# Performance work log

Hardware: AMD Instinct MI355X
Metric: run time of the kernel (lower is better)

## Reference

```python
import jax, jax.numpy as jnp
import numpy as np

A = 5.0  # smoothness parameter 'a'

def setup_inputs() -> dict:
    key = jax.random.key(0)
    kx, kw = jax.random.split(key)
    x = jax.random.uniform(kx, (1024, 512), dtype=jnp.float32)
    weight = jax.random.uniform(kw, (512, 512), dtype=jnp.float32)
    return {"x": x, "weight": weight}

def reference(x, weight):
    # inner: [batch, in, out] broadcast min
    inner = jnp.minimum(x[..., None], weight[None])
    # smooth union (smooth max) over the 'in' dim: logsumexp(a*z)/a
    smooth = jax.scipy.special.logsumexp(A * inner, axis=-2) / A
    hard = jnp.max(inner, axis=-2)
    # straight-through: forward value = hard, gradient flows through smooth
    return jax.lax.stop_gradient(hard - smooth) + smooth
```

## Files before the change

kernel.cpp:

```cpp
#include <hip/hip_runtime.h>


typedef _Float16 h2 __attribute__((ext_vector_type(2)));
typedef unsigned int uint32;

#define MDIM 1024
#define KDIM 512
#define NDIM 512
#define K2   (KDIM / 2)
#define MB   8
#define NT   256
#define NWAVE 8
#define KP   (K2 / NWAVE)

__device__ __forceinline__ uint32 pkmin(uint32 a, uint32 b) {
    uint32 d;
    asm("v_pk_min_f16 %0, %1, %2" : "=v"(d) : "v"(a), "v"(b));
    return d;
}
__device__ __forceinline__ uint32 pkmax(uint32 a, uint32 b) {
    uint32 d;
    asm("v_pk_max_f16 %0, %1, %2" : "=v"(d) : "v"(a), "v"(b));
    return d;
}

__global__ __launch_bounds__(512) void pack_f16(const float* __restrict__ x,
                                                const float* __restrict__ w,
                                                uint32* __restrict__ xp,
                                                uint32* __restrict__ wp)
{
    const int b = blockIdx.x, tid = threadIdx.x;
    if (b < 256) {
        const int idx = b * 512 + tid;
        const int k2 = idx >> 9, n = idx & 511;
        h2 v;
        v[0] = (_Float16)w[(size_t)(2 * k2) * NDIM + n];
        v[1] = (_Float16)w[(size_t)(2 * k2 + 1) * NDIM + n];
        wp[idx] = __builtin_bit_cast(uint32, v);
    } else {
        const int idx = (b - 256) * 512 + tid;
        const float2 f = ((const float2*)x)[idx];
        h2 v;
        v[0] = (_Float16)f.x;
        v[1] = (_Float16)f.y;
        xp[idx] = __builtin_bit_cast(uint32, v);
    }
}

__global__ __launch_bounds__(512, 2) void tropical_r16(
    const uint32* __restrict__ xp,
    const uint32* __restrict__ wp,
    float* __restrict__ out)
{
    const int tid  = threadIdx.x;
    const int lane = tid & 63;
    const int wv   = tid >> 6;
    const int m0   = blockIdx.x * MB;
    const int n0   = blockIdx.y * NT;
    const int kp0  = __builtin_amdgcn_readfirstlane(wv * KP);

    __shared__ float red[NWAVE][MB][NT];

    const uint4* __restrict__ wb =
        (const uint4*)(wp + (size_t)kp0 * NDIM + n0) + lane;
    const uint32* __restrict__ xr0 = xp + (size_t)m0 * K2 + kp0;

    uint32 acc[MB][4];
#pragma unroll
    for (int r = 0; r < MB; ++r)
#pragma unroll
        for (int j = 0; j < 4; ++j) acc[r][j] = 0u;

    uint4 A = wb[0], B = wb[(size_t)128];

#pragma unroll 2
    for (int i = 0; i < KP; ++i) {
        uint4 C;
        if (i + 2 < KP) C = wb[(size_t)(i + 2) * 128];
#pragma unroll
        for (int r = 0; r < MB; ++r) {
            const uint32 xv = xr0[(size_t)r * K2 + i];
            acc[r][0] = pkmax(acc[r][0], pkmin(xv, A.x));
            acc[r][1] = pkmax(acc[r][1], pkmin(xv, A.y));
            acc[r][2] = pkmax(acc[r][2], pkmin(xv, A.z));
            acc[r][3] = pkmax(acc[r][3], pkmin(xv, A.w));
        }
        A = B; B = C;
    }

#pragma unroll
    for (int r = 0; r < MB; ++r) {
        float4 v;
        {
            h2 a0 = __builtin_bit_cast(h2, acc[r][0]);
            h2 a1 = __builtin_bit_cast(h2, acc[r][1]);
            h2 a2 = __builtin_bit_cast(h2, acc[r][2]);
            h2 a3 = __builtin_bit_cast(h2, acc[r][3]);
            v.x = fmaxf((float)a0[0], (float)a0[1]);
            v.y = fmaxf((float)a1[0], (float)a1[1]);
            v.z = fmaxf((float)a2[0], (float)a2[1]);
            v.w = fmaxf((float)a3[0], (float)a3[1]);
        }
        ((float4*)&red[wv][r][0])[lane] = v;
    }
    __syncthreads();

    {
        const int r  = tid >> 6;
        const int c4 = tid & 63;
        float4 v = ((const float4*)&red[0][r][0])[c4];
#pragma unroll
        for (int q = 1; q < NWAVE; ++q) {
            float4 u = ((const float4*)&red[q][r][0])[c4];
            v.x = fmaxf(v.x, u.x); v.y = fmaxf(v.y, u.y);
            v.z = fmaxf(v.z, u.z); v.w = fmaxf(v.w, u.w);
        }
        *(float4*)(out + (size_t)(m0 + r) * NDIM + n0 + 4 * c4) = v;
    }
}

extern "C" void kernel_launch(void* const* d_in, const int* in_sizes, int n_in,
                              void* d_out, int out_size, void* d_ws, size_t ws_size,
                              hipStream_t stream) {
    const float* x = (const float*)d_in[0];
    const float* w = (const float*)d_in[1];
    float* out = (float*)d_out;

    uint32* xp = (uint32*)d_ws;
    uint32* wp = xp + (size_t)MDIM * K2;

    pack_f16<<<dim3(768), dim3(512), 0, stream>>>(x, w, xp, wp);
    tropical_r16<<<dim3(MDIM / MB, NDIM / NT), dim3(512), 0, stream>>>(xp, wp, out);
}
```

Before: 72.14 us.

## Transpose packed x for contiguous scalar loads and retile to 16x128 blocks

The pack kernel now writes the f16-packed x in k-major order. This lets each block read a contiguous run of 16 rows per k step through uniform scalar loads, and the inline asm forces the x operand of v_pk_min_f16 into an SGPR. The output tile changes from 8 rows by 256 columns to 16 rows by 128 columns, so each lane holds 2 packed columns instead of 4. The goal is fewer weight bytes per x value and cheaper wide scalar x fetches. In exchange, the transposing pack reads x with a large stride and is uncoalesced, which adds cost to the pre-pass.

Result: slower. 74.76 us (+3.6%).

```diff
diff --git a/kernel.cpp b/kernel.cpp
--- a/kernel.cpp
+++ b/kernel.cpp
@@ -7,15 +7,15 @@
 #define MDIM 1024
 #define KDIM 512
 #define NDIM 512
-#define K2   (KDIM / 2)
-#define MB   8
-#define NT   256
+#define K2   256
+#define MB   16
+#define NT   128
 #define NWAVE 8
-#define KP   (K2 / NWAVE)
+#define KP   32
 
-__device__ __forceinline__ uint32 pkmin(uint32 a, uint32 b) {
+__device__ __forceinline__ uint32 pkmin_sv(uint32 s, uint32 v) {
     uint32 d;
-    asm("v_pk_min_f16 %0, %1, %2" : "=v"(d) : "v"(a), "v"(b));
+    asm("v_pk_min_f16 %0, %1, %2" : "=v"(d) : "s"(s), "v"(v));
     return d;
 }
 __device__ __forceinline__ uint32 pkmax(uint32 a, uint32 b) {
@@ -24,10 +24,10 @@
     return d;
 }
 
-__global__ __launch_bounds__(512) void pack_f16(const float* __restrict__ x,
-                                                const float* __restrict__ w,
-                                                uint32* __restrict__ xp,
-                                                uint32* __restrict__ wp)
+__global__ __launch_bounds__(512) void pack_t(const float* __restrict__ x,
+                                              const float* __restrict__ w,
+                                              uint32* __restrict__ xpT,
+                                              uint32* __restrict__ wp)
 {
     const int b = blockIdx.x, tid = threadIdx.x;
     if (b < 256) {
@@ -39,16 +39,17 @@
         wp[idx] = __builtin_bit_cast(uint32, v);
     } else {
         const int idx = (b - 256) * 512 + tid;
-        const float2 f = ((const float2*)x)[idx];
+        const int k2 = idx >> 10, m = idx & 1023;
+        const float2 f = ((const float2*)x)[(size_t)m * K2 + k2];
         h2 v;
         v[0] = (_Float16)f.x;
         v[1] = (_Float16)f.y;
-        xp[idx] = __builtin_bit_cast(uint32, v);
+        xpT[idx] = __builtin_bit_cast(uint32, v);
     }
 }
 
-__global__ __launch_bounds__(512, 2) void tropical_r16(
-    const uint32* __restrict__ xp,
+__global__ __launch_bounds__(512, 2) void tropical_r17(
+    const uint32* __restrict__ xpT,
     const uint32* __restrict__ wp,
     float* __restrict__ out)
 {
@@ -61,53 +62,44 @@
 
     __shared__ float red[NWAVE][MB][NT];
 
-    const uint4* __restrict__ wb =
-        (const uint4*)(wp + (size_t)kp0 * NDIM + n0) + lane;
-    const uint32* __restrict__ xr0 = xp + (size_t)m0 * K2 + kp0;
+    const uint32* __restrict__ xs = xpT + (size_t)kp0 * MDIM + m0;
+    const uint2* __restrict__ wb2 =
+        (const uint2*)(wp + (size_t)kp0 * NDIM + n0) + lane;
 
-    uint32 acc[MB][4];
+    uint32 acc[MB][2];
 #pragma unroll
-    for (int r = 0; r < MB; ++r)
-#pragma unroll
-        for (int j = 0; j < 4; ++j) acc[r][j] = 0u;
+    for (int r = 0; r < MB; ++r) { acc[r][0] = 0u; acc[r][1] = 0u; }
 
-    uint4 A = wb[0], B = wb[(size_t)128];
+    uint2 A = wb2[0], B = wb2[256];
 
 #pragma unroll 2
     for (int i = 0; i < KP; ++i) {
-        uint4 C;
-        if (i + 2 < KP) C = wb[(size_t)(i + 2) * 128];
+        uint2 C;
+        if (i + 2 < KP) C = wb2[(size_t)(i + 2) * 256];
+        const uint32* __restrict__ xr = xs + (size_t)i * MDIM;
 #pragma unroll
         for (int r = 0; r < MB; ++r) {
-            const uint32 xv = xr0[(size_t)r * K2 + i];
-            acc[r][0] = pkmax(acc[r][0], pkmin(xv, A.x));
-            acc[r][1] = pkmax(acc[r][1], pkmin(xv, A.y));
-            acc[r][2] = pkmax(acc[r][2], pkmin(xv, A.z));
-            acc[r][3] = pkmax(acc[r][3], pkmin(xv, A.w));
+            const uint32 xv = xr[r];
+            acc[r][0] = pkmax(acc[r][0], pkmin_sv(xv, A.x));
+            acc[r][1] = pkmax(acc[r][1], pkmin_sv(xv, A.y));
         }
         A = B; B = C;
     }
 
 #pragma unroll
     for (int r = 0; r < MB; ++r) {
-        float4 v;
-        {
-            h2 a0 = __builtin_bit_cast(h2, acc[r][0]);
-            h2 a1 = __builtin_bit_cast(h2, acc[r][1]);
-            h2 a2 = __builtin_bit_cast(h2, acc[r][2]);
-            h2 a3 = __builtin_bit_cast(h2, acc[r][3]);
-            v.x = fmaxf((float)a0[0], (float)a0[1]);
-            v.y = fmaxf((float)a1[0], (float)a1[1]);
-            v.z = fmaxf((float)a2[0], (float)a2[1]);
-            v.w = fmaxf((float)a3[0], (float)a3[1]);
-        }
-        ((float4*)&red[wv][r][0])[lane] = v;
+        h2 a0 = __builtin_bit_cast(h2, acc[r][0]);
+        h2 a1 = __builtin_bit_cast(h2, acc[r][1]);
+        float2 v;
+        v.x = fmaxf((float)a0[0], (float)a0[1]);
+        v.y = fmaxf((float)a1[0], (float)a1[1]);
+        ((float2*)&red[wv][r][0])[lane] = v;
     }
     __syncthreads();
 
     {
-        const int r  = tid >> 6;
-        const int c4 = tid & 63;
+        const int r  = tid >> 5;
+        const int c4 = tid & 31;
         float4 v = ((const float4*)&red[0][r][0])[c4];
 #pragma unroll
         for (int q = 1; q < NWAVE; ++q) {
@@ -126,9 +118,9 @@
     const float* w = (const float*)d_in[1];
     float* out = (float*)d_out;
 
-    uint32* xp = (uint32*)d_ws;
-    uint32* wp = xp + (size_t)MDIM * K2;
+    uint32* xpT = (uint32*)d_ws;
+    uint32* wp  = xpT + (size_t)K2 * MDIM;
 
-    pack_f16<<<dim3(768), dim3(512), 0, stream>>>(x, w, xp, wp);
-    tropical_r16<<<dim3(MDIM / MB, NDIM / NT), dim3(512), 0, stream>>>(xp, wp, out);
+    pack_t<<<dim3(768), dim3(512), 0, stream>>>(x, w, xpT, wp);
+    tropical_r17<<<dim3(MDIM / MB, NDIM / NT), dim3(512), 0, stream>>>(xpT, wp, out);
 }
```

## Fuse fp16 packing into tropical kernel, reading fp32 inputs directly

Applied to the files above, without the earlier changes.

Drops the separate pack_f16 kernel and converts fp32 x and weight to packed fp16 inside the main min-max loop using v_cvt_pk_f16_f32. This removes one kernel launch and a global write/read round trip of the packed buffers. In exchange each block loads twice as many bytes of weight and x, and does redundant conversions in the inner loop across blocks.

Result: no change. 72.10 us (-0.1%).

```diff
diff --git a/kernel.cpp b/kernel.cpp
--- a/kernel.cpp
+++ b/kernel.cpp
@@ -7,11 +7,10 @@
 #define MDIM 1024
 #define KDIM 512
 #define NDIM 512
-#define K2   (KDIM / 2)
-#define MB   8
-#define NT   256
+#define MB 8
+#define NT 256
+#define KW 64
 #define NWAVE 8
-#define KP   (K2 / NWAVE)
 
 __device__ __forceinline__ uint32 pkmin(uint32 a, uint32 b) {
     uint32 d;
@@ -23,33 +22,15 @@
     asm("v_pk_max_f16 %0, %1, %2" : "=v"(d) : "v"(a), "v"(b));
     return d;
 }
-
-__global__ __launch_bounds__(512) void pack_f16(const float* __restrict__ x,
-                                                const float* __restrict__ w,
-                                                uint32* __restrict__ xp,
-                                                uint32* __restrict__ wp)
-{
-    const int b = blockIdx.x, tid = threadIdx.x;
-    if (b < 256) {
-        const int idx = b * 512 + tid;
-        const int k2 = idx >> 9, n = idx & 511;
-        h2 v;
-        v[0] = (_Float16)w[(size_t)(2 * k2) * NDIM + n];
-        v[1] = (_Float16)w[(size_t)(2 * k2 + 1) * NDIM + n];
-        wp[idx] = __builtin_bit_cast(uint32, v);
-    } else {
-        const int idx = (b - 256) * 512 + tid;
-        const float2 f = ((const float2*)x)[idx];
-        h2 v;
-        v[0] = (_Float16)f.x;
-        v[1] = (_Float16)f.y;
-        xp[idx] = __builtin_bit_cast(uint32, v);
-    }
+__device__ __forceinline__ uint32 cvt_pk(float lo, float hi) {
+    uint32 d;
+    asm("v_cvt_pk_f16_f32 %0, %1, %2" : "=v"(d) : "v"(lo), "v"(hi));
+    return d;
 }
 
-__global__ __launch_bounds__(512, 2) void tropical_r16(
-    const uint32* __restrict__ xp,
-    const uint32* __restrict__ wp,
+__global__ __launch_bounds__(512, 2) void tropical_r18(
+    const float* __restrict__ x,
+    const float* __restrict__ w,
     float* __restrict__ out)
 {
     const int tid  = threadIdx.x;
@@ -57,13 +38,13 @@
     const int wv   = tid >> 6;
     const int m0   = blockIdx.x * MB;
     const int n0   = blockIdx.y * NT;
-    const int kp0  = __builtin_amdgcn_readfirstlane(wv * KP);
+    const int k0   = __builtin_amdgcn_readfirstlane(wv * KW);
 
     __shared__ float red[NWAVE][MB][NT];
 
-    const uint4* __restrict__ wb =
-        (const uint4*)(wp + (size_t)kp0 * NDIM + n0) + lane;
-    const uint32* __restrict__ xr0 = xp + (size_t)m0 * K2 + kp0;
+    const float4* __restrict__ wf =
+        (const float4*)(w + (size_t)k0 * NDIM + n0) + lane;
+    const float* __restrict__ xs = x + (size_t)m0 * KDIM + k0;
 
     uint32 acc[MB][4];
 #pragma unroll
@@ -71,36 +52,44 @@
 #pragma unroll
         for (int j = 0; j < 4; ++j) acc[r][j] = 0u;
 
-    uint4 A = wb[0], B = wb[(size_t)128];
+    float4 A0 = wf[0], A1 = wf[128];
+    float4 B0 = wf[256], B1 = wf[384];
 
 #pragma unroll 2
-    for (int i = 0; i < KP; ++i) {
-        uint4 C;
-        if (i + 2 < KP) C = wb[(size_t)(i + 2) * 128];
+    for (int i = 0; i < KW / 2; ++i) {
+        float4 C0, C1;
+        if (i + 2 < KW / 2) {
+            C0 = wf[(size_t)(2 * i + 4) * 128];
+            C1 = wf[(size_t)(2 * i + 5) * 128];
+        }
+        const uint32 w0 = cvt_pk(A0.x, A1.x);
+        const uint32 w1 = cvt_pk(A0.y, A1.y);
+        const uint32 w2 = cvt_pk(A0.z, A1.z);
+        const uint32 w3 = cvt_pk(A0.w, A1.w);
 #pragma unroll
         for (int r = 0; r < MB; ++r) {
-            const uint32 xv = xr0[(size_t)r * K2 + i];
-            acc[r][0] = pkmax(acc[r][0], pkmin(xv, A.x));
-            acc[r][1] = pkmax(acc[r][1], pkmin(xv, A.y));
-            acc[r][2] = pkmax(acc[r][2], pkmin(xv, A.z));
-            acc[r][3] = pkmax(acc[r][3], pkmin(xv, A.w));
+            const float xl = xs[(size_t)r * KDIM + 2 * i];
+            const float xh = xs[(size_t)r * KDIM + 2 * i + 1];
+            const uint32 xv = cvt_pk(xl, xh);
+            acc[r][0] = pkmax(acc[r][0], pkmin(xv, w0));
+            acc[r][1] = pkmax(acc[r][1], pkmin(xv, w1));
+            acc[r][2] = pkmax(acc[r][2], pkmin(xv, w2));
+            acc[r][3] = pkmax(acc[r][3], pkmin(xv, w3));
         }
-        A = B; B = C;
+        A0 = B0; A1 = B1; B0 = C0; B1 = C1;
     }
 
 #pragma unroll
     for (int r = 0; r < MB; ++r) {
+        h2 a0 = __builtin_bit_cast(h2, acc[r][0]);
+        h2 a1 = __builtin_bit_cast(h2, acc[r][1]);
+        h2 a2 = __builtin_bit_cast(h2, acc[r][2]);
+        h2 a3 = __builtin_bit_cast(h2, acc[r][3]);
         float4 v;
-        {
-            h2 a0 = __builtin_bit_cast(h2, acc[r][0]);
-            h2 a1 = __builtin_bit_cast(h2, acc[r][1]);
-            h2 a2 = __builtin_bit_cast(h2, acc[r][2]);
-            h2 a3 = __builtin_bit_cast(h2, acc[r][3]);
-            v.x = fmaxf((float)a0[0], (float)a0[1]);
-            v.y = fmaxf((float)a1[0], (float)a1[1]);
-            v.z = fmaxf((float)a2[0], (float)a2[1]);
-            v.w = fmaxf((float)a3[0], (float)a3[1]);
-        }
+        v.x = fmaxf((float)a0[0], (float)a0[1]);
+        v.y = fmaxf((float)a1[0], (float)a1[1]);
+        v.z = fmaxf((float)a2[0], (float)a2[1]);
+        v.w = fmaxf((float)a3[0], (float)a3[1]);
         ((float4*)&red[wv][r][0])[lane] = v;
     }
     __syncthreads();
@@ -126,9 +115,6 @@
     const float* w = (const float*)d_in[1];
     float* out = (float*)d_out;
 
-    uint32* xp = (uint32*)d_ws;
-    uint32* wp = xp + (size_t)MDIM * K2;
-
-    pack_f16<<<dim3(768), dim3(512), 0, stream>>>(x, w, xp, wp);
-    tropical_r16<<<dim3(MDIM / MB, NDIM / NT), dim3(512), 0, stream>>>(xp, wp, out);
+    dim3 grid(MDIM / MB, NDIM / NT);
+    tropical_r18<<<grid, dim3(512), 0, stream>>>(x, w, out);
 }
```
